# Kernel optimization log

Measured on AMD Instinct MI355X. Metric: run time of the kernel, lower is better.

Reference implementation:

```python
import jax, jax.numpy as jnp
import numpy as np

N = 50000
E = 800000
IN_DIM = 6
HID = 32
HEADS = 2
NEG_SLOPE = 0.2


def setup_inputs() -> dict:
    key = jax.random.key(0)
    ks = jax.random.split(key, 12)
    x = jax.random.normal(ks[0], (N, IN_DIM), dtype=jnp.float32)
    edge_index = jax.random.randint(ks[1], (2, E), 0, N, dtype=jnp.int64)
    s = 0.1
    W1 = jax.random.normal(ks[2], (IN_DIM, HEADS * HID), jnp.float32) * s
    a_src1 = jax.random.normal(ks[3], (HEADS, HID), jnp.float32) * s
    a_dst1 = jax.random.normal(ks[4], (HEADS, HID), jnp.float32) * s
    b1 = jnp.zeros((HEADS * HID,), jnp.float32)
    W2 = jax.random.normal(ks[5], (HEADS * HID, HID), jnp.float32) * s
    a_src2 = jax.random.normal(ks[6], (1, HID), jnp.float32) * s
    a_dst2 = jax.random.normal(ks[7], (1, HID), jnp.float32) * s
    b2 = jnp.zeros((HID,), jnp.float32)
    Wout = jax.random.normal(ks[8], (HID, 1), jnp.float32) * s
    bout = jnp.zeros((1,), jnp.float32)
    return {"x": x, "edge_index": edge_index, "W1": W1, "a_src1": a_src1,
            "a_dst1": a_dst1, "b1": b1, "W2": W2, "a_src2": a_src2,
            "a_dst2": a_dst2, "b2": b2, "Wout": Wout, "bout": bout}


def gat_conv(x, src, dst, n, W, a_src, a_dst, b, heads, out_ch, concat):
    # x: [N, F_in]; src/dst: [E'] (self-loops already appended)
    h = (x @ W).reshape(n, heads, out_ch)              # [N, H, C]
    alpha_s = jnp.sum(h * a_src, axis=-1)              # [N, H]
    alpha_d = jnp.sum(h * a_dst, axis=-1)              # [N, H]
    e = jax.nn.leaky_relu(alpha_s[src] + alpha_d[dst], NEG_SLOPE)  # [E', H]
    # segment softmax over incoming edges of each destination node
    m = jax.ops.segment_max(e, dst, num_segments=n)    # [N, H]
    ex = jnp.exp(e - m[dst])
    denom = jax.ops.segment_sum(ex, dst, num_segments=n)
    alpha = ex / denom[dst]                            # [E', H]
    out = jax.ops.segment_sum(alpha[:, :, None] * h[src], dst, num_segments=n)  # [N, H, C]
    out = out.reshape(n, heads * out_ch) if concat else out.mean(axis=1)
    return out + b


def reference(x, edge_index, W1, a_src1, a_dst1, b1, W2, a_src2, a_dst2, b2, Wout, bout):
    n = x.shape[0]
    loops = jnp.arange(n, dtype=edge_index.dtype)
    src = jnp.concatenate([edge_index[0], loops])
    dst = jnp.concatenate([edge_index[1], loops])
    h = jax.nn.relu(gat_conv(x, src, dst, n, W1, a_src1, a_dst1, b1, HEADS, HID, True))
    h = jax.nn.relu(gat_conv(h, src, dst, n, W2, a_src2, a_dst2, b2, 1, HID, False))
    return jax.nn.sigmoid(h @ Wout + bout).squeeze(-1)  # [N]
```

## Files before the change

kernel.cpp:

```cpp
#include <hip/hip_runtime.h>
#include <hip/hip_fp16.h>

#define N_NODES 50000
#define N_EDGES 800000
#define ETOT    (N_EDGES + N_NODES)
#define NEG_SLOPE 0.2f
#define NBIN    ((N_NODES + 255) / 256)
#define CHUNK   4096
#define B_COARSE ((ETOT + CHUNK - 1) / CHUNK)
#define G_NODE1 ((N_NODES + 3) / 4)

__device__ __forceinline__ float leaky(float v) {
    return v > 0.f ? v : NEG_SLOPE * v;
}

__device__ __forceinline__ void edge_src_dst(const int* ei, int e, int& src, int& dst) {
    if (e < N_EDGES) { src = ei[e]; dst = ei[N_EDGES + e]; }
    else             { src = dst = e - N_EDGES; }
}

__global__ void k_pre(const float* __restrict__ x, const float* __restrict__ W1,
                      const float* __restrict__ a_src1, const float* __restrict__ a_dst1,
                      float* __restrict__ as1, float* __restrict__ ad1,
                      const int* __restrict__ ei, int* __restrict__ bh) {
    __shared__ int h[NBIN];
    if (blockIdx.x < G_NODE1) {
        int node = blockIdx.x * 4 + (threadIdx.x >> 6);
        if (node >= N_NODES) return;
        int j = threadIdx.x & 63;
        int head = j >> 5;
        float hv = 0.f;
#pragma unroll
        for (int k = 0; k < 6; ++k)
            hv += x[node * 6 + k] * W1[k * 64 + j];
        float s = hv * a_src1[j];
        float d = hv * a_dst1[j];
#pragma unroll
        for (int m = 1; m < 32; m <<= 1) {
            s += __shfl_xor(s, m);
            d += __shfl_xor(d, m);
        }
        if ((j & 31) == 0) {
            as1[node * 2 + head] = s;
            ad1[node * 2 + head] = d;
        }
    } else {
        int b = blockIdx.x - G_NODE1;
        for (int i = threadIdx.x; i < NBIN; i += 256) h[i] = 0;
        __syncthreads();
        int base = b * CHUNK;
        int lim = min(base + CHUNK, ETOT);
        for (int e = base + threadIdx.x; e < lim; e += 256) {
            int s, d; edge_src_dst(ei, e, s, d);
            atomicAdd(&h[d >> 8], 1);
        }
        __syncthreads();
        for (int i = threadIdx.x; i < NBIN; i += 256)
            bh[b * NBIN + i] = h[i];
    }
}

__global__ void k_cscan(int* __restrict__ bh, int* __restrict__ binoff) {
    __shared__ int s[256];
    int t = threadIdx.x;
    int run = 0;
    if (t < NBIN) {
        for (int b = 0; b < B_COARSE; ++b) {
            int v = bh[b * NBIN + t];
            bh[b * NBIN + t] = run;
            run += v;
        }
    }
    int v = (t < NBIN) ? run : 0;
    int x = v;
    s[t] = x;
    __syncthreads();
#pragma unroll
    for (int o = 1; o < 256; o <<= 1) {
        int tt = (t >= o) ? s[t - o] : 0;
        __syncthreads();
        x += tt;
        s[t] = x;
        __syncthreads();
    }
    if (t < NBIN) binoff[t] = x - v;
    if (t == 255) binoff[NBIN] = x;
}

__global__ void k_cscatter(const int* __restrict__ ei, const int* __restrict__ bh,
                           const int* __restrict__ binoff, unsigned* __restrict__ ebin) {
    __shared__ int cur[NBIN];
    for (int i = threadIdx.x; i < NBIN; i += 256)
        cur[i] = bh[blockIdx.x * NBIN + i] + binoff[i];
    __syncthreads();
    int base = blockIdx.x * CHUNK;
    int lim = min(base + CHUNK, ETOT);
    for (int e = base + threadIdx.x; e < lim; e += 256) {
        int s, d; edge_src_dst(ei, e, s, d);
        int pos = atomicAdd(&cur[d >> 8], 1);
        ebin[pos] = ((unsigned)s << 8) | (unsigned)(d & 255);
    }
}

__global__ void k_fine(const unsigned* __restrict__ ebin, const int* __restrict__ binoff,
                       int* __restrict__ rowstart, int* __restrict__ csr_src) {
    __shared__ int h[256];
    __shared__ int cur[256];
    int bin = blockIdx.x;
    int beg = binoff[bin], end = binoff[bin + 1];
    int t = threadIdx.x;
    h[t] = 0;
    __syncthreads();
    for (int i = beg + t; i < end; i += 256)
        atomicAdd(&h[ebin[i] & 255u], 1);
    __syncthreads();
    int v = h[t];
    int x = v;
    cur[t] = x;
    __syncthreads();
#pragma unroll
    for (int o = 1; o < 256; o <<= 1) {
        int tt = (t >= o) ? cur[t - o] : 0;
        __syncthreads();
        x += tt;
        cur[t] = x;
        __syncthreads();
    }
    int start = beg + x - v;
    int node = bin * 256 + t;
    if (node < N_NODES) rowstart[node] = start;
    if (bin == NBIN - 1 && t == 0) rowstart[N_NODES] = ETOT;
    cur[t] = start;
    __syncthreads();
    for (int i = beg + t; i < end; i += 256) {
        unsigned p = ebin[i];
        int pos = atomicAdd(&cur[p & 255u], 1);
        csr_src[pos] = (int)(p >> 8);
    }
}

__global__ void k_gat1(const int* __restrict__ csr_src, const int* __restrict__ rowstart,
                       const float* __restrict__ as1, const float* __restrict__ ad1,
                       const float* __restrict__ x, const float* __restrict__ W1,
                       const float* __restrict__ b1, float* __restrict__ o1) {
    int node = blockIdx.x * 16 + (threadIdx.x >> 4);
    if (node >= N_NODES) return;
    int l = threadIdx.x & 15;

    float p[4][6];
    float bv[4];
#pragma unroll
    for (int m = 0; m < 4; ++m) {
        int c = l + 16 * m;
#pragma unroll
        for (int k = 0; k < 6; ++k)
            p[m][k] = W1[k * 64 + c];
        bv[m] = b1[c];
    }

    int beg = rowstart[node], end = rowstart[node + 1];
    float2 adv = ((const float2*)ad1)[node];

    float a0 = 0, a1 = 0, a2 = 0, a3 = 0, a4 = 0, a5 = 0;
    float c0 = 0, c1 = 0, c2 = 0, c3 = 0, c4 = 0, c5 = 0;
    float dp0 = 0, dp1 = 0;
    for (int i = beg + l; i < end; i += 16) {
        int s = csr_src[i];
        float2 aa = ((const float2*)as1)[s];
        float w0 = __expf(leaky(aa.x + adv.x));
        float w1 = __expf(leaky(aa.y + adv.y));
        dp0 += w0;
        dp1 += w1;
        const float2* xs = (const float2*)(x + s * 6);
        float2 u = xs[0], v = xs[1], w = xs[2];
        a0 += w0 * u.x; a1 += w0 * u.y; a2 += w0 * v.x;
        a3 += w0 * v.y; a4 += w0 * w.x; a5 += w0 * w.y;
        c0 += w1 * u.x; c1 += w1 * u.y; c2 += w1 * v.x;
        c3 += w1 * v.y; c4 += w1 * w.x; c5 += w1 * w.y;
    }
#pragma unroll
    for (int o = 8; o; o >>= 1) {
        a0 += __shfl_xor(a0, o); a1 += __shfl_xor(a1, o); a2 += __shfl_xor(a2, o);
        a3 += __shfl_xor(a3, o); a4 += __shfl_xor(a4, o); a5 += __shfl_xor(a5, o);
        c0 += __shfl_xor(c0, o); c1 += __shfl_xor(c1, o); c2 += __shfl_xor(c2, o);
        c3 += __shfl_xor(c3, o); c4 += __shfl_xor(c4, o); c5 += __shfl_xor(c5, o);
        dp0 += __shfl_xor(dp0, o); dp1 += __shfl_xor(dp1, o);
    }
    float inv0 = 1.f / dp0;
    float inv1 = 1.f / dp1;
    float* ob = o1 + (size_t)node * 64;
#pragma unroll
    for (int m = 0; m < 4; ++m) {
        float dot;
        if (m < 2)
            dot = a0 * p[m][0] + a1 * p[m][1] + a2 * p[m][2]
                + a3 * p[m][3] + a4 * p[m][4] + a5 * p[m][5];
        else
            dot = c0 * p[m][0] + c1 * p[m][1] + c2 * p[m][2]
                + c3 * p[m][3] + c4 * p[m][4] + c5 * p[m][5];
        float v = dot * (m < 2 ? inv0 : inv1) + bv[m];
        ob[l + 16 * m] = v > 0.f ? v : 0.f;
    }
}

__global__ void k_node2(const float* __restrict__ o1, const float* __restrict__ W2,
                        const float* __restrict__ a_src2, const float* __restrict__ a_dst2,
                        __half* __restrict__ h2h, float* __restrict__ as2,
                        float* __restrict__ ad2) {
    __shared__ float W2s[64 * 32];
    for (int i = threadIdx.x; i < 64 * 32; i += 256)
        W2s[i] = W2[i];
    __syncthreads();

    int node = blockIdx.x * 8 + (threadIdx.x >> 5);
    if (node >= N_NODES) return;
    int j = threadIdx.x & 31;

    float acc = 0.f;
#pragma unroll
    for (int k = 0; k < 64; ++k)
        acc += o1[node * 64 + k] * W2s[k * 32 + j];
    h2h[node * 32 + j] = __float2half(acc);

    float s = acc * a_src2[j];
    float d = acc * a_dst2[j];
#pragma unroll
    for (int m = 1; m < 32; m <<= 1) {
        s += __shfl_xor(s, m, 32);
        d += __shfl_xor(d, m, 32);
    }
    if (j == 0) {
        as2[node] = s;
        ad2[node] = d;
    }
}

__global__ void k_gat2(const int* __restrict__ csr_src, const int* __restrict__ rowstart,
                       const float* __restrict__ as2, const float* __restrict__ ad2,
                       const __half2* __restrict__ h2h, const float* __restrict__ b2,
                       const float* __restrict__ Wout, const float* __restrict__ bout,
                       float* __restrict__ out) {
    int node = blockIdx.x * 4 + (threadIdx.x >> 6);
    if (node >= N_NODES) return;
    int j = threadIdx.x & 63;
    int f = j & 15;
    int slot = j >> 4;
    int beg = rowstart[node], end = rowstart[node + 1];
    float adv = ad2[node];

    float accx = 0.f, accy = 0.f, dp = 0.f;
    for (int base = beg; base < end; base += 64) {
        int idx = base + j;
        float w = 0.f;
        int s = 0;
        if (idx < end) {
            s = csr_src[idx];
            w = __expf(leaky(as2[s] + adv));
            dp += w;
        }
        int cnt = min(64, end - base);
        for (int k = 0; k < cnt; k += 4) {
            int   sk = __shfl(s, k + slot);
            float wk = __shfl(w, k + slot);
            float2 hv = __half22float2(h2h[sk * 16 + f]);
            accx += wk * hv.x;
            accy += wk * hv.y;
        }
    }
#pragma unroll
    for (int o = 32; o; o >>= 1)
        dp += __shfl_xor(dp, o);
    accx += __shfl_xor(accx, 16); accy += __shfl_xor(accy, 16);
    accx += __shfl_xor(accx, 32); accy += __shfl_xor(accy, 32);

    float inv = 1.f / dp;
    float vx = accx * inv + b2[2 * f];
    float vy = accy * inv + b2[2 * f + 1];
    vx = vx > 0.f ? vx : 0.f;
    vy = vy > 0.f ? vy : 0.f;
    float t = vx * Wout[2 * f] + vy * Wout[2 * f + 1];
#pragma unroll
    for (int o = 8; o; o >>= 1)
        t += __shfl_xor(t, o);
    if (j == 0)
        out[node] = 1.f / (1.f + __expf(-(t + bout[0])));
}

extern "C" void kernel_launch(void* const* d_in, const int* in_sizes, int n_in,
                              void* d_out, int out_size, void* d_ws, size_t ws_size,
                              hipStream_t stream) {
    const float* x    = (const float*)d_in[0];
    const int*   ei   = (const int*)  d_in[1];
    const float* W1   = (const float*)d_in[2];
    const float* asw1 = (const float*)d_in[3];
    const float* adw1 = (const float*)d_in[4];
    const float* b1   = (const float*)d_in[5];
    const float* W2   = (const float*)d_in[6];
    const float* asw2 = (const float*)d_in[7];
    const float* adw2 = (const float*)d_in[8];
    const float* b2   = (const float*)d_in[9];
    const float* Wout = (const float*)d_in[10];
    const float* bout = (const float*)d_in[11];
    float* out = (float*)d_out;

    char* p = (char*)d_ws;
    auto carve = [&](size_t bytes) {
        void* r = (void*)p;
        p += (bytes + 255) & ~size_t(255);
        return r;
    };
    float*    o1       = (float*)   carve((size_t)N_NODES * 64 * 4);
    __half*   h2h      = (__half*)  carve((size_t)N_NODES * 32 * 2);
    float*    as1      = (float*)   carve((size_t)N_NODES * 2 * 4);
    float*    ad1      = (float*)   carve((size_t)N_NODES * 2 * 4);
    float*    as2      = (float*)   carve((size_t)N_NODES * 4);
    float*    ad2      = (float*)   carve((size_t)N_NODES * 4);
    int*      bh       = (int*)     carve((size_t)B_COARSE * NBIN * 4);
    int*      binoff   = (int*)     carve((size_t)(NBIN + 1) * 4);
    unsigned* ebin     = (unsigned*)carve((size_t)ETOT * 4);
    int*      rowstart = (int*)     carve((size_t)(N_NODES + 1) * 4);
    int*      csr_src  = (int*)     carve((size_t)ETOT * 4);

    const int TB = 256;

    k_pre     <<<G_NODE1 + B_COARSE, TB, 0, stream>>>(x, W1, asw1, adw1, as1, ad1, ei, bh);
    k_cscan   <<<1, TB, 0, stream>>>(bh, binoff);
    k_cscatter<<<B_COARSE, TB, 0, stream>>>(ei, bh, binoff, ebin);
    k_fine    <<<NBIN, TB, 0, stream>>>(ebin, binoff, rowstart, csr_src);

    k_gat1 <<<(N_NODES + 15) / 16, TB, 0, stream>>>(csr_src, rowstart, as1, ad1, x, W1, b1, o1);

    k_node2<<<(N_NODES + 7) / 8, TB, 0, stream>>>(o1, W2, asw2, adw2, h2h, as2, ad2);
    k_gat2 <<<(N_NODES + 3) / 4, TB, 0, stream>>>(csr_src, rowstart, as2, ad2,
                                                  (const __half2*)h2h, b2, Wout, bout, out);
}
```

Baseline: 106.8 us.

## Fuse layer-1 aggregation with layer-2 node transform via shared memory

Merges the GAT layer-1 aggregation kernel and the layer-2 linear/attention-coefficient kernel into one. Each block stages its 16 nodes' 64-wide layer-1 outputs in shared memory and immediately multiplies them by W2 held in shared memory. This removes the o1 global round trip (a 12.8 MB write and read) and one kernel launch. In exchange, every block loads W2 into shared memory and adds a block barrier, and the early return is dropped, relying on N being divisible by 16.

```diff
diff --git a/kernel.cpp b/kernel.cpp
--- a/kernel.cpp
+++ b/kernel.cpp
@@ -9,6 +9,7 @@
 #define CHUNK   4096
 #define B_COARSE ((ETOT + CHUNK - 1) / CHUNK)
 #define G_NODE1 ((N_NODES + 3) / 4)
+#define NG1     (N_NODES / 16)
 
 __device__ __forceinline__ float leaky(float v) {
     return v > 0.f ? v : NEG_SLOPE * v;
@@ -139,13 +140,22 @@
     }
 }
 
-__global__ void k_gat1(const int* __restrict__ csr_src, const int* __restrict__ rowstart,
-                       const float* __restrict__ as1, const float* __restrict__ ad1,
-                       const float* __restrict__ x, const float* __restrict__ W1,
-                       const float* __restrict__ b1, float* __restrict__ o1) {
-    int node = blockIdx.x * 16 + (threadIdx.x >> 4);
-    if (node >= N_NODES) return;
-    int l = threadIdx.x & 15;
+__global__ void k_gat12(const int* __restrict__ csr_src, const int* __restrict__ rowstart,
+                        const float* __restrict__ as1, const float* __restrict__ ad1,
+                        const float* __restrict__ x, const float* __restrict__ W1,
+                        const float* __restrict__ b1, const float* __restrict__ W2,
+                        const float* __restrict__ as_w2, const float* __restrict__ ad_w2,
+                        __half* __restrict__ h2h, float* __restrict__ as2,
+                        float* __restrict__ ad2) {
+    __shared__ float W2s[64 * 32];
+    __shared__ float o1s[16 * 66];
+    int t = threadIdx.x;
+    for (int i = t; i < 64 * 32; i += 256)
+        W2s[i] = W2[i];
+
+    int l = t & 15;
+    int ln = t >> 4;
+    int node = blockIdx.x * 16 + ln;
 
     float p[4][6];
     float bv[4];
@@ -188,7 +198,6 @@
     }
     float inv0 = 1.f / dp0;
     float inv1 = 1.f / dp1;
-    float* ob = o1 + (size_t)node * 64;
 #pragma unroll
     for (int m = 0; m < 4; ++m) {
         float dot;
@@ -199,39 +208,29 @@
             dot = c0 * p[m][0] + c1 * p[m][1] + c2 * p[m][2]
                 + c3 * p[m][3] + c4 * p[m][4] + c5 * p[m][5];
         float v = dot * (m < 2 ? inv0 : inv1) + bv[m];
-        ob[l + 16 * m] = v > 0.f ? v : 0.f;
-    }
-}
-
-__global__ void k_node2(const float* __restrict__ o1, const float* __restrict__ W2,
-                        const float* __restrict__ a_src2, const float* __restrict__ a_dst2,
-                        __half* __restrict__ h2h, float* __restrict__ as2,
-                        float* __restrict__ ad2) {
-    __shared__ float W2s[64 * 32];
-    for (int i = threadIdx.x; i < 64 * 32; i += 256)
-        W2s[i] = W2[i];
-    __syncthreads();
-
-    int node = blockIdx.x * 8 + (threadIdx.x >> 5);
-    if (node >= N_NODES) return;
-    int j = threadIdx.x & 31;
-
-    float acc = 0.f;
-#pragma unroll
-    for (int k = 0; k < 64; ++k)
-        acc += o1[node * 64 + k] * W2s[k * 32 + j];
-    h2h[node * 32 + j] = __float2half(acc);
-
-    float s = acc * a_src2[j];
-    float d = acc * a_dst2[j];
-#pragma unroll
-    for (int m = 1; m < 32; m <<= 1) {
-        s += __shfl_xor(s, m, 32);
-        d += __shfl_xor(d, m, 32);
-    }
-    if (j == 0) {
-        as2[node] = s;
-        ad2[node] = d;
+        o1s[ln * 66 + l + 16 * m] = v > 0.f ? v : 0.f;
+    }
+    __syncthreads();
+
+    float h0 = 0.f, h1 = 0.f;
+#pragma unroll
+    for (int k = 0; k < 64; ++k) {
+        float ov = o1s[ln * 66 + k];
+        h0 += ov * W2s[k * 32 + l];
+        h1 += ov * W2s[k * 32 + l + 16];
+    }
+    h2h[node * 32 + l] = __float2half(h0);
+    h2h[node * 32 + l + 16] = __float2half(h1);
+    float s2 = h0 * as_w2[l] + h1 * as_w2[l + 16];
+    float d2 = h0 * ad_w2[l] + h1 * ad_w2[l + 16];
+#pragma unroll
+    for (int o = 8; o; o >>= 1) {
+        s2 += __shfl_xor(s2, o);
+        d2 += __shfl_xor(d2, o);
+    }
+    if (l == 0) {
+        as2[node] = s2;
+        ad2[node] = d2;
     }
 }
 
@@ -309,7 +308,6 @@
         p += (bytes + 255) & ~size_t(255);
         return r;
     };
-    float*    o1       = (float*)   carve((size_t)N_NODES * 64 * 4);
     __half*   h2h      = (__half*)  carve((size_t)N_NODES * 32 * 2);
     float*    as1      = (float*)   carve((size_t)N_NODES * 2 * 4);
     float*    ad1      = (float*)   carve((size_t)N_NODES * 2 * 4);
@@ -328,9 +326,9 @@
     k_cscatter<<<B_COARSE, TB, 0, stream>>>(ei, bh, binoff, ebin);
     k_fine    <<<NBIN, TB, 0, stream>>>(ebin, binoff, rowstart, csr_src);
 
-    k_gat1 <<<(N_NODES + 15) / 16, TB, 0, stream>>>(csr_src, rowstart, as1, ad1, x, W1, b1, o1);
-
-    k_node2<<<(N_NODES + 7) / 8, TB, 0, stream>>>(o1, W2, asw2, adw2, h2h, as2, ad2);
+    k_gat12<<<NG1, TB, 0, stream>>>(csr_src, rowstart, as1, ad1, x, W1, b1,
+                                    W2, asw2, adw2, h2h, as2, ad2);
+
     k_gat2 <<<(N_NODES + 3) / 4, TB, 0, stream>>>(csr_src, rowstart, as2, ad2,
                                                   (const __half2*)h2h, b2, Wout, bout, out);
 }
```

Measured after the change: 98.66 us (median of 2 runs). 1.08x faster.
